# Kernel tuning notes

Hardware: AMD Instinct MI355X
Metric: run time of the kernel (lower is better)

Reference implementation:

```python
import jax, jax.numpy as jnp
import numpy as np

B, N, D = 16, 4096, 768   # bags, instances per bag, feature dim
H, L, K = 12, 2, 16       # heads, MHA layers, topk
DH = D // H               # head dim (also gate hidden dim)


def _ln(x, g, b, eps=1e-5):
    m = x.mean(-1, keepdims=True)
    v = x.var(-1, keepdims=True)
    return (x - m) / jnp.sqrt(v + eps) * g + b


def setup_inputs() -> dict:
    key = jax.random.key(0)
    ks = jax.random.split(key, 8)
    s = 0.02
    return {
        "x": jax.random.normal(ks[0], (B, N, D), jnp.float32),
        "cls_token": jax.random.normal(ks[1], (1, 1, D), jnp.float32),
        "ln_g": jnp.ones((D,), jnp.float32),
        "ln_b": jnp.zeros((D,), jnp.float32),
        "gln_g": jnp.ones((D,), jnp.float32),
        "gln_b": jnp.zeros((D,), jnp.float32),
        "gW1": jax.random.normal(ks[2], (DH, D), jnp.float32) * s,
        "gb1": jnp.zeros((DH,), jnp.float32),
        "gW2": jax.random.normal(ks[3], (1, DH), jnp.float32) * s,
        "gb2": jnp.zeros((1,), jnp.float32),
        "Wqkv": jax.random.normal(ks[4], (L, 3 * D, D), jnp.float32) * s,
        "bqkv": jnp.zeros((L, 3 * D), jnp.float32),
        "Wo": jax.random.normal(ks[5], (L, D, D), jnp.float32) * s,
        "bo": jnp.zeros((L, D), jnp.float32),
    }


def reference(x, cls_token, ln_g, ln_b, gln_g, gln_b, gW1, gb1, gW2, gb2, Wqkv, bqkv, Wo, bo):
    # --- per-bag attention gate: LN -> Linear(D,DH) -> GELU -> Linear(DH,1) -> sigmoid ---
    z = _ln(x, gln_g, gln_b)                                      # [B,N,D]
    h = jax.nn.gelu(jnp.einsum('bnd,ed->bne', z, gW1) + gb1, approximate=False)
    w = jax.nn.sigmoid((jnp.einsum('bne,oe->bno', h, gW2) + gb2)[..., 0])  # [B,N]
    # --- top-k selection (argsort descending, take first K) + gather + weight ---
    topv, topi = jax.lax.top_k(w, K)                              # [B,K]
    sel = jnp.take_along_axis(x, topi[..., None], axis=1) * topv[..., None]  # [B,K,D]
    # --- prepend cls token, shared LayerNorm ---
    cls = jnp.broadcast_to(cls_token, (B, 1, D))
    seq = jnp.concatenate([cls, sel], axis=1)                     # [B,K+1,D]
    z0 = _ln(seq, ln_g, ln_b)
    a = z0
    S = K + 1
    scale = 1.0 / jnp.sqrt(jnp.asarray(DH, jnp.float32))
    # --- stacked MHA; residual always from z0, shared ln (matches source) ---
    for l in range(L):
        qkv = jnp.einsum('bsd,ed->bse', a, Wqkv[l]) + bqkv[l]     # [B,S,3D]
        q, k, v = jnp.split(qkv, 3, axis=-1)
        q = q.reshape(B, S, H, DH)
        k = k.reshape(B, S, H, DH)
        v = v.reshape(B, S, H, DH)
        att = jax.nn.softmax(jnp.einsum('bqhd,bkhd->bhqk', q, k) * scale, axis=-1)
        o = jnp.einsum('bhqk,bkhd->bqhd', att, v).reshape(B, S, D)
        o = jnp.einsum('bsd,ed->bse', o, Wo[l]) + bo[l]
        a = _ln(z0 + o, ln_g, ln_b)
    # dropout is identity in eval mode
    return a[:, 0, :]                                             # [B,D]
```

## Files before the change

### kernel.cpp

```cpp
#include <hip/hip_runtime.h>
#include <hip/hip_bf16.h>
#include <math.h>

#define B_   16
#define N_   4096
#define D_   768
#define H_   12
#define L_   2
#define K_   16
#define S_   17
#define M_   272
#define BN_  65536

typedef __bf16 bf16x8 __attribute__((ext_vector_type(8)));
typedef float  f32x4  __attribute__((ext_vector_type(4)));

static __device__ __forceinline__ unsigned short f2bf(float f) {
    __bf16 h = (__bf16)f;
    return __builtin_bit_cast(unsigned short, h);
}
static __device__ __forceinline__ float bf2f(unsigned short u) {
    __bf16 h = __builtin_bit_cast(__bf16, u);
    return (float)h;
}
static __device__ __forceinline__ unsigned long long umax64(unsigned long long a, unsigned long long b) {
    return a > b ? a : b;
}
static __device__ __forceinline__ void split4(const float4& v, ushort4& hh, ushort4& ll) {
    hh.x = f2bf(v.x); ll.x = f2bf(v.x - bf2f(hh.x));
    hh.y = f2bf(v.y); ll.y = f2bf(v.y - bf2f(hh.y));
    hh.z = f2bf(v.z); ll.z = f2bf(v.z - bf2f(hh.z));
    hh.w = f2bf(v.w); ll.w = f2bf(v.w - bf2f(hh.w));
}

__global__ __launch_bounds__(256)
void gate_kernel(const float* __restrict__ x, const float* __restrict__ gln_g,
                 const float* __restrict__ gln_b, const float* __restrict__ gW1,
                 const float* __restrict__ gb1, const float* __restrict__ gW2,
                 const float* __restrict__ gb2, float* __restrict__ wbuf)
{
    __shared__ __align__(16) char WS[16384];
    __shared__ float mS[128], rS[128], A1s[64], A2s[64];
    __shared__ float rA1[256], rA2[256];
    char* WhB = WS;
    char* WlB = WS + 8192;

    const int t   = threadIdx.x;
    const int bn0 = blockIdx.x * 128;
    const int wv  = t >> 6, la = t & 63, fr = la & 15, fq = la >> 4;

    const int te = t >> 2;
    const int tq = (t & 3) * 16;
    const float* wrow = gW1 + (size_t)te * D_ + tq;

    const float* arow0 = x + (size_t)(bn0 + wv * 32 + fr) * D_;
    const float* arow1 = arow0 + (size_t)16 * D_;

    f32x4 acc[2][4];
    #pragma unroll
    for (int mi = 0; mi < 2; ++mi)
        #pragma unroll
        for (int ni = 0; ni < 4; ++ni) {
            f32x4 z = {0.f, 0.f, 0.f, 0.f};
            acc[mi][ni] = z;
        }

    float sx0 = 0.f, sxx0 = 0.f, sx1 = 0.f, sxx1 = 0.f;
    float a1p = 0.f, a2p = 0.f;

    float4 pa[2][2][2];
    #pragma unroll
    for (int mi = 0; mi < 2; ++mi) {
        const float* ar = mi ? arow1 : arow0;
        #pragma unroll
        for (int ks = 0; ks < 2; ++ks) {
            pa[mi][ks][0] = *(const float4*)(ar + ks * 32 + fq * 8);
            pa[mi][ks][1] = *(const float4*)(ar + ks * 32 + fq * 8 + 4);
        }
    }

    for (int kt = 0; kt < 12; ++kt) {
        __syncthreads();
        {
            const float* wsrc = wrow + kt * 64;
            const float* gsrc = gln_g + kt * 64 + tq;
            const float* bsrc = gln_b + kt * 64 + tq;
            #pragma unroll
            for (int j = 0; j < 4; ++j) {
                float4 w4 = *(const float4*)(wsrc + j * 4);
                float4 g4 = *(const float4*)(gsrc + j * 4);
                float4 b4 = *(const float4*)(bsrc + j * 4);
                float4 wt;
                wt.x = w4.x * g4.x; wt.y = w4.y * g4.y;
                wt.z = w4.z * g4.z; wt.w = w4.w * g4.w;
                a1p += wt.x + wt.y + wt.z + wt.w;
                a2p += b4.x * w4.x + b4.y * w4.y + b4.z * w4.z + b4.w * w4.w;
                ushort4 hh, ll;
                split4(wt, hh, ll);
                int byte = (te * 128 + (tq + j * 4) * 2) ^ ((te & 7) << 4);
                *(ushort4*)(WhB + byte) = hh;
                *(ushort4*)(WlB + byte) = ll;
            }
        }
        __syncthreads();

        float4 na[2][2][2];
        if (kt < 11) {
            #pragma unroll
            for (int mi = 0; mi < 2; ++mi) {
                const float* ar = (mi ? arow1 : arow0) + (kt + 1) * 64;
                #pragma unroll
                for (int ks = 0; ks < 2; ++ks) {
                    na[mi][ks][0] = *(const float4*)(ar + ks * 32 + fq * 8);
                    na[mi][ks][1] = *(const float4*)(ar + ks * 32 + fq * 8 + 4);
                }
            }
        }

        #pragma unroll
        for (int ks = 0; ks < 2; ++ks) {
            bf16x8 ah[2], al[2];
            #pragma unroll
            for (int mi = 0; mi < 2; ++mi) {
                float v[8];
                v[0] = pa[mi][ks][0].x; v[1] = pa[mi][ks][0].y;
                v[2] = pa[mi][ks][0].z; v[3] = pa[mi][ks][0].w;
                v[4] = pa[mi][ks][1].x; v[5] = pa[mi][ks][1].y;
                v[6] = pa[mi][ks][1].z; v[7] = pa[mi][ks][1].w;
                #pragma unroll
                for (int i = 0; i < 8; ++i) {
                    if (mi == 0) { sx0 += v[i]; sxx0 += v[i] * v[i]; }
                    else         { sx1 += v[i]; sxx1 += v[i] * v[i]; }
                    __bf16 h = (__bf16)v[i];
                    ah[mi][i] = h;
                    al[mi][i] = (__bf16)(v[i] - (float)h);
                }
            }
            bf16x8 bh[4], bl[4];
            const int kb = ks * 64 + fq * 16;
            #pragma unroll
            for (int ni = 0; ni < 4; ++ni) {
                int e    = ni * 16 + fr;
                int byte = (e * 128 + kb) ^ ((e & 7) << 4);
                bh[ni] = *(const bf16x8*)(WhB + byte);
                bl[ni] = *(const bf16x8*)(WlB + byte);
            }
            #pragma unroll
            for (int mi = 0; mi < 2; ++mi)
                #pragma unroll
                for (int ni = 0; ni < 4; ++ni) {
                    acc[mi][ni] = __builtin_amdgcn_mfma_f32_16x16x32_bf16(ah[mi], bh[ni], acc[mi][ni], 0, 0, 0);
                    acc[mi][ni] = __builtin_amdgcn_mfma_f32_16x16x32_bf16(ah[mi], bl[ni], acc[mi][ni], 0, 0, 0);
                    acc[mi][ni] = __builtin_amdgcn_mfma_f32_16x16x32_bf16(al[mi], bh[ni], acc[mi][ni], 0, 0, 0);
                }
        }
        if (kt < 11) {
            #pragma unroll
            for (int mi = 0; mi < 2; ++mi)
                #pragma unroll
                for (int ks = 0; ks < 2; ++ks) {
                    pa[mi][ks][0] = na[mi][ks][0];
                    pa[mi][ks][1] = na[mi][ks][1];
                }
        }
    }

    __syncthreads();
    {
        float s0 = sx0, q0 = sxx0, s1 = sx1, q1 = sxx1;
        s0 += __shfl_xor(s0, 16); s0 += __shfl_xor(s0, 32);
        q0 += __shfl_xor(q0, 16); q0 += __shfl_xor(q0, 32);
        s1 += __shfl_xor(s1, 16); s1 += __shfl_xor(s1, 32);
        q1 += __shfl_xor(q1, 16); q1 += __shfl_xor(q1, 32);
        if (fq == 0) {
            int r0 = wv * 32 + fr;
            float m0 = s0 * (1.0f / D_);
            mS[r0] = m0;
            rS[r0] = rsqrtf(q0 * (1.0f / D_) - m0 * m0 + 1e-5f);
            float m1 = s1 * (1.0f / D_);
            mS[r0 + 16] = m1;
            rS[r0 + 16] = rsqrtf(q1 * (1.0f / D_) - m1 * m1 + 1e-5f);
        }
    }
    rA1[te * 4 + (t & 3)] = a1p;
    rA2[te * 4 + (t & 3)] = a2p;
    __syncthreads();
    if (t < 64) {
        A1s[t] = rA1[t * 4] + rA1[t * 4 + 1] + rA1[t * 4 + 2] + rA1[t * 4 + 3];
        A2s[t] = rA2[t * 4] + rA2[t * 4 + 1] + rA2[t * 4 + 2] + rA2[t * 4 + 3];
    }
    __syncthreads();

    float w2v[4], a1v[4], a2b[4];
    #pragma unroll
    for (int ni = 0; ni < 4; ++ni) {
        int e = ni * 16 + fr;
        w2v[ni] = gW2[e];
        a1v[ni] = A1s[e];
        a2b[ni] = A2s[e] + gb1[e];
    }
    float gb2v = gb2[0];

    #pragma unroll
    for (int mi = 0; mi < 2; ++mi) {
        #pragma unroll
        for (int j = 0; j < 4; ++j) {
            int inst = wv * 32 + mi * 16 + fq * 4 + j;
            float m = mS[inst], rs = rS[inst];
            float tp = 0.f;
            #pragma unroll
            for (int ni = 0; ni < 4; ++ni) {
                float h  = rs * (acc[mi][ni][j] - m * a1v[ni]) + a2b[ni];
                float hg = 0.5f * h * (1.0f + erff(h * 0.70710678118654752f));
                tp = fmaf(hg, w2v[ni], tp);
            }
            tp += __shfl_xor(tp, 1);
            tp += __shfl_xor(tp, 2);
            tp += __shfl_xor(tp, 4);
            tp += __shfl_xor(tp, 8);
            if (fr == 0) wbuf[bn0 + inst] = 1.0f / (1.0f + expf(-(tp + gb2v)));
        }
    }
}

__global__ __launch_bounds__(256)
void topkbuild_kernel(const float* __restrict__ x, const float* __restrict__ cls,
                      const float* __restrict__ ln_g, const float* __restrict__ ln_b,
                      const float* __restrict__ wbuf, float* __restrict__ z0)
{
    __shared__ unsigned long long SB[40];
    __shared__ float sm[8];
    const int b = blockIdx.x, t = threadIdx.x;
    const int la = t & 63, wid = t >> 6;

    unsigned long long key[16];
    #pragma unroll
    for (int j = 0; j < 16; ++j) {
        int i = t + 256 * j;
        float v = wbuf[(size_t)b * N_ + i];
        key[j] = ((unsigned long long)__float_as_uint(v) << 12) | (unsigned long long)(4095 - i);
    }
    for (int k = 0; k < K_; ++k) {
        unsigned long long kk = key[0];
        #pragma unroll
        for (int j = 1; j < 16; ++j) kk = umax64(kk, key[j]);
        #pragma unroll
        for (int o = 1; o < 64; o <<= 1) kk = umax64(kk, (unsigned long long)__shfl_xor(kk, o));
        if (la == 0) SB[wid] = kk;
        __syncthreads();
        if (t == 0) {
            unsigned long long m = umax64(umax64(SB[0], SB[1]), umax64(SB[2], SB[3]));
            SB[8] = m;
            SB[16 + k] = m;
        }
        __syncthreads();
        unsigned long long m = SB[8];
        int wi = 4095 - (int)(m & 0xfffULL);
        #pragma unroll
        for (int j = 0; j < 16; ++j)
            if (wi == t + 256 * j) key[j] = 0ULL;
        __syncthreads();
    }

    for (int s = 0; s < S_; ++s) {
        float v[3];
        if (s == 0) {
            #pragma unroll
            for (int p = 0; p < 3; ++p) v[p] = cls[t + 256 * p];
        } else {
            unsigned long long m = SB[16 + s - 1];
            int   idx = 4095 - (int)(m & 0xfffULL);
            float tv  = __uint_as_float((unsigned int)(m >> 12));
            const float* row = &x[((size_t)b * N_ + idx) * D_];
            #pragma unroll
            for (int p = 0; p < 3; ++p) v[p] = row[t + 256 * p] * tv;
        }
        float sum = 0.f, ss = 0.f;
        #pragma unroll
        for (int p = 0; p < 3; ++p) { sum += v[p]; ss += v[p] * v[p]; }
        #pragma unroll
        for (int o = 32; o; o >>= 1) { sum += __shfl_down(sum, o); ss += __shfl_down(ss, o); }
        if (la == 0) { sm[wid * 2] = sum; sm[wid * 2 + 1] = ss; }
        __syncthreads();
        sum = sm[0] + sm[2] + sm[4] + sm[6];
        ss  = sm[1] + sm[3] + sm[5] + sm[7];
        __syncthreads();
        float m = sum * (1.0f / D_), rstd = rsqrtf(ss * (1.0f / D_) - m * m + 1e-5f);
        #pragma unroll
        for (int p = 0; p < 3; ++p) {
            int d = t + 256 * p;
            z0[((size_t)(b * S_ + s)) * D_ + d] = (v[p] - m) * rstd * ln_g[d] + ln_b[d];
        }
    }
}

__global__ __launch_bounds__(256)
void gemm_mfma(const float* __restrict__ A, const float* __restrict__ W,
               const float* __restrict__ bias, float* __restrict__ C, int N)
{
    __shared__ __align__(16) char SB[32768];
    char* AhB = SB;
    char* AlB = SB + 8192;
    char* WhB = SB + 16384;
    char* WlB = SB + 24576;

    const int t  = threadIdx.x;
    const int m0 = blockIdx.x * 64, n0 = blockIdx.y * 64;

    const int sr = t >> 2;
    const int sc = (t & 3) * 16;
    const int gm = m0 + sr;
    const bool aok = (gm < M_);
    const float* asrc = A + (size_t)gm * D_ + sc;
    const float* wsrc = W + (size_t)(n0 + sr) * D_ + sc;

    const int wv = t >> 6, la = t & 63;
    const int fr = la & 15, fq = la >> 4;
    const int wm = (wv & 1) * 32, wn = (wv >> 1) * 32;

    f32x4 acc[2][2];
    #pragma unroll
    for (int mi = 0; mi < 2; ++mi)
        #pragma unroll
        for (int ni = 0; ni < 2; ++ni) {
            f32x4 z = {0.f, 0.f, 0.f, 0.f};
            acc[mi][ni] = z;
        }

    float4 pa[4], pw[4];
    #pragma unroll
    for (int q = 0; q < 4; ++q) {
        pa[q] = aok ? *(const float4*)(asrc + q * 4) : make_float4(0.f, 0.f, 0.f, 0.f);
        pw[q] = *(const float4*)(wsrc + q * 4);
    }

    const int abyte0 = sr * 128 + sc * 2;
    const int asw0   = (abyte0)      ^ ((sr & 7) << 4);
    const int asw1   = (abyte0 + 16) ^ ((sr & 7) << 4);

    for (int kt = 0; kt < 12; ++kt) {
        __syncthreads();
        {
            ushort4 hh[4], ll[4];
            #pragma unroll
            for (int q = 0; q < 4; ++q) split4(pa[q], hh[q], ll[q]);
            *(ushort4*)(AhB + asw0)     = hh[0];
            *(ushort4*)(AhB + asw0 + 8) = hh[1];
            *(ushort4*)(AhB + asw1)     = hh[2];
            *(ushort4*)(AhB + asw1 + 8) = hh[3];
            *(ushort4*)(AlB + asw0)     = ll[0];
            *(ushort4*)(AlB + asw0 + 8) = ll[1];
            *(ushort4*)(AlB + asw1)     = ll[2];
            *(ushort4*)(AlB + asw1 + 8) = ll[3];
            #pragma unroll
            for (int q = 0; q < 4; ++q) split4(pw[q], hh[q], ll[q]);
            *(ushort4*)(WhB + asw0)     = hh[0];
            *(ushort4*)(WhB + asw0 + 8) = hh[1];
            *(ushort4*)(WhB + asw1)     = hh[2];
            *(ushort4*)(WhB + asw1 + 8) = hh[3];
            *(ushort4*)(WlB + asw0)     = ll[0];
            *(ushort4*)(WlB + asw0 + 8) = ll[1];
            *(ushort4*)(WlB + asw1)     = ll[2];
            *(ushort4*)(WlB + asw1 + 8) = ll[3];
        }
        __syncthreads();
        if (kt < 11) {
            const float* an  = asrc + (kt + 1) * 64;
            const float* wn2 = wsrc + (kt + 1) * 64;
            #pragma unroll
            for (int q = 0; q < 4; ++q) {
                pa[q] = aok ? *(const float4*)(an + q * 4) : make_float4(0.f, 0.f, 0.f, 0.f);
                pw[q] = *(const float4*)(wn2 + q * 4);
            }
        }
        #pragma unroll
        for (int ks = 0; ks < 2; ++ks) {
            int kb = ks * 64 + fq * 16;
            bf16x8 ah[2], al[2], bh[2], bl[2];
            #pragma unroll
            for (int mi = 0; mi < 2; ++mi) {
                int r    = wm + mi * 16 + fr;
                int byte = (r * 128 + kb) ^ ((r & 7) << 4);
                ah[mi] = *(const bf16x8*)(AhB + byte);
                al[mi] = *(const bf16x8*)(AlB + byte);
            }
            #pragma unroll
            for (int ni = 0; ni < 2; ++ni) {
                int r    = wn + ni * 16 + fr;
                int byte = (r * 128 + kb) ^ ((r & 7) << 4);
                bh[ni] = *(const bf16x8*)(WhB + byte);
                bl[ni] = *(const bf16x8*)(WlB + byte);
            }
            #pragma unroll
            for (int mi = 0; mi < 2; ++mi)
                #pragma unroll
                for (int ni = 0; ni < 2; ++ni) {
                    acc[mi][ni] = __builtin_amdgcn_mfma_f32_16x16x32_bf16(ah[mi], bh[ni], acc[mi][ni], 0, 0, 0);
                    acc[mi][ni] = __builtin_amdgcn_mfma_f32_16x16x32_bf16(ah[mi], bl[ni], acc[mi][ni], 0, 0, 0);
                    acc[mi][ni] = __builtin_amdgcn_mfma_f32_16x16x32_bf16(al[mi], bh[ni], acc[mi][ni], 0, 0, 0);
                }
        }
    }

    #pragma unroll
    for (int mi = 0; mi < 2; ++mi) {
        #pragma unroll
        for (int j = 0; j < 4; ++j) {
            int m = m0 + wm + mi * 16 + fq * 4 + j;
            if (m < M_) {
                #pragma unroll
                for (int ni = 0; ni < 2; ++ni) {
                    int n = n0 + wn + ni * 16 + fr;
                    C[(size_t)m * N + n] = acc[mi][ni][j] + bias[n];
                }
            }
        }
    }
}

__global__ __launch_bounds__(256)
void attn_kernel(const float* __restrict__ qkvb, float* __restrict__ obuf)
{
    __shared__ __align__(16) float F[3 * S_ * 65 + S_ * 18];
    float* qs  = F;
    float* ks  = F + S_ * 65;
    float* vs  = F + 2 * S_ * 65;
    float* att = F + 3 * S_ * 65;
    const int bh = blockIdx.x, b = bh / H_, h = bh % H_;
    const int bq = b * S_;
    const int t = threadIdx.x;

    for (int idx = t; idx < S_ * 64; idx += 256) {
        int s = idx >> 6, d = idx & 63;
        size_t off = (size_t)(bq + s) * (3 * D_) + h * 64 + d;
        qs[s * 65 + d] = qkvb[off];
        ks[s * 65 + d] = qkvb[off + D_];
        vs[s * 65 + d] = qkvb[off + 2 * D_];
    }
    __syncthreads();
    for (int idx = t; idx < S_ * S_; idx += 256) {
        int i = idx / S_, j = idx % S_;
        float sdot = 0.f;
        #pragma unroll
        for (int d = 0; d < 64; ++d) sdot = fmaf(qs[i * 65 + d], ks[j * 65 + d], sdot);
        att[i * 18 + j] = sdot * 0.125f;
    }
    __syncthreads();
    if (t < S_) {
        float mx = -1e30f;
        for (int j = 0; j < S_; ++j) mx = fmaxf(mx, att[t * 18 + j]);
        float ssum = 0.f;
        for (int j = 0; j < S_; ++j) { float e = expf(att[t * 18 + j] - mx); att[t * 18 + j] = e; ssum += e; }
        float inv = 1.0f / ssum;
        for (int j = 0; j < S_; ++j) att[t * 18 + j] *= inv;
    }
    __syncthreads();
    for (int idx = t; idx < S_ * 64; idx += 256) {
        int i = idx >> 6, d = idx & 63;
        float s = 0.f;
        #pragma unroll
        for (int j = 0; j < S_; ++j) s = fmaf(att[i * 18 + j], vs[j * 65 + d], s);
        obuf[(size_t)(bq + i) * D_ + h * 64 + d] = s;
    }
}

__global__ __launch_bounds__(256)
void resln_kernel(const float* __restrict__ z0, const float* __restrict__ projb,
                  const float* __restrict__ ln_g, const float* __restrict__ ln_b,
                  float* __restrict__ abuf)
{
    __shared__ float sm[8];
    const int r = blockIdx.x, t = threadIdx.x;
    float v[3];
    #pragma unroll
    for (int p = 0; p < 3; ++p) {
        int d = t + 256 * p;
        v[p] = z0[(size_t)r * D_ + d] + projb[(size_t)r * D_ + d];
    }
    float sum = 0.f, ss = 0.f;
    #pragma unroll
    for (int p = 0; p < 3; ++p) { sum += v[p]; ss += v[p] * v[p]; }
    #pragma unroll
    for (int o = 32; o; o >>= 1) { sum += __shfl_down(sum, o); ss += __shfl_down(ss, o); }
    int wid = t >> 6, la = t & 63;
    if (la == 0) { sm[wid * 2] = sum; sm[wid * 2 + 1] = ss; }
    __syncthreads();
    sum = sm[0] + sm[2] + sm[4] + sm[6];
    ss  = sm[1] + sm[3] + sm[5] + sm[7];
    float m = sum * (1.0f / D_), rstd = rsqrtf(ss * (1.0f / D_) - m * m + 1e-5f);
    #pragma unroll
    for (int p = 0; p < 3; ++p) {
        int d = t + 256 * p;
        abuf[(size_t)r * D_ + d] = (v[p] - m) * rstd * ln_g[d] + ln_b[d];
    }
}

__global__ __launch_bounds__(256)
void outln_kernel(const float* __restrict__ z0, const float* __restrict__ projb,
                  const float* __restrict__ ln_g, const float* __restrict__ ln_b,
                  float* __restrict__ out)
{
    __shared__ float sm[8];
    const int b = blockIdx.x, t = threadIdx.x;
    const size_t r = (size_t)b * S_;
    float v[3];
    #pragma unroll
    for (int p = 0; p < 3; ++p) {
        int d = t + 256 * p;
        v[p] = z0[r * D_ + d] + projb[r * D_ + d];
    }
    float sum = 0.f, ss = 0.f;
    #pragma unroll
    for (int p = 0; p < 3; ++p) { sum += v[p]; ss += v[p] * v[p]; }
    #pragma unroll
    for (int o = 32; o; o >>= 1) { sum += __shfl_down(sum, o); ss += __shfl_down(ss, o); }
    int wid = t >> 6, la = t & 63;
    if (la == 0) { sm[wid * 2] = sum; sm[wid * 2 + 1] = ss; }
    __syncthreads();
    sum = sm[0] + sm[2] + sm[4] + sm[6];
    ss  = sm[1] + sm[3] + sm[5] + sm[7];
    float m = sum * (1.0f / D_), rstd = rsqrtf(ss * (1.0f / D_) - m * m + 1e-5f);
    #pragma unroll
    for (int p = 0; p < 3; ++p) {
        int d = t + 256 * p;
        out[(size_t)b * D_ + d] = (v[p] - m) * rstd * ln_g[d] + ln_b[d];
    }
}

extern "C" void kernel_launch(void* const* d_in, const int* in_sizes, int n_in,
                              void* d_out, int out_size, void* d_ws, size_t ws_size,
                              hipStream_t stream)
{
    const float* x     = (const float*)d_in[0];
    const float* cls   = (const float*)d_in[1];
    const float* ln_g  = (const float*)d_in[2];
    const float* ln_b  = (const float*)d_in[3];
    const float* gln_g = (const float*)d_in[4];
    const float* gln_b = (const float*)d_in[5];
    const float* gW1   = (const float*)d_in[6];
    const float* gb1   = (const float*)d_in[7];
    const float* gW2   = (const float*)d_in[8];
    const float* gb2   = (const float*)d_in[9];
    const float* Wqkv  = (const float*)d_in[10];
    const float* bqkv  = (const float*)d_in[11];
    const float* Wo    = (const float*)d_in[12];
    const float* bo    = (const float*)d_in[13];
    float* out = (float*)d_out;

    float* ws    = (float*)d_ws;
    float* wbuf  = ws;
    float* z0    = ws + BN_;
    float* abuf  = z0 + (size_t)M_ * D_;
    float* qkvb  = abuf + (size_t)M_ * D_;
    float* obuf  = qkvb + (size_t)M_ * 3 * D_;
    float* projb = obuf + (size_t)M_ * D_;

    gate_kernel<<<BN_ / 128, 256, 0, stream>>>(x, gln_g, gln_b, gW1, gb1, gW2, gb2, wbuf);
    topkbuild_kernel<<<B_, 256, 0, stream>>>(x, cls, ln_g, ln_b, wbuf, z0);

    gemm_mfma<<<dim3(5, 36), 256, 0, stream>>>(z0, Wqkv, bqkv, qkvb, 3 * D_);
    attn_kernel<<<B_ * H_, 256, 0, stream>>>(qkvb, obuf);
    gemm_mfma<<<dim3(5, 12), 256, 0, stream>>>(obuf, Wo, bo, projb, D_);
    resln_kernel<<<M_, 256, 0, stream>>>(z0, projb, ln_g, ln_b, abuf);

    gemm_mfma<<<dim3(5, 36), 256, 0, stream>>>(abuf, Wqkv + (size_t)3 * D_ * D_,
                                               bqkv + 3 * D_, qkvb, 3 * D_);
    attn_kernel<<<B_ * H_, 256, 0, stream>>>(qkvb, obuf);
    gemm_mfma<<<dim3(5, 12), 256, 0, stream>>>(obuf, Wo + (size_t)D_ * D_, bo + D_, projb, D_);
    outln_kernel<<<B_, 256, 0, stream>>>(z0, projb, ln_g, ln_b, out);
}
```

Baseline: 171.4 us.

## Precompute gate weight split once and compute only CLS row in final layer

A new single-block prep kernel folds the gate LayerNorm gamma into gW1, splits the result into bf16 hi/lo pairs in a global swizzled layout, and reduces the A1/A2 bias terms once. Before, each of 512 gate blocks redid this conversion for every k-tile, and the gate kernel now just copies the prepared tiles into LDS. In the last layer only the CLS query row goes through attention, and a small 16-row projection kernel replaces the full Wo GEMM, since only a[:,0,:] is returned. The cost is an extra tiny kernel launch, plus the second-layer QKV GEMM still computing all rows.

```diff
diff --git a/kernel.cpp b/kernel.cpp
--- a/kernel.cpp
+++ b/kernel.cpp
@@ -34,25 +34,50 @@
 }
 
 __global__ __launch_bounds__(256)
-void gate_kernel(const float* __restrict__ x, const float* __restrict__ gln_g,
-                 const float* __restrict__ gln_b, const float* __restrict__ gW1,
+void prep_kernel(const float* __restrict__ gln_g, const float* __restrict__ gln_b,
+                 const float* __restrict__ gW1,
+                 char* __restrict__ wsh, char* __restrict__ wsl,
+                 float* __restrict__ A1g, float* __restrict__ A2g)
+{
+    const int t = threadIdx.x;
+    const int e = t >> 2;
+    const int c0 = (t & 3) * 192;
+    float a1 = 0.f, a2 = 0.f;
+    for (int c = c0; c < c0 + 192; c += 4) {
+        float4 w = *(const float4*)&gW1[(size_t)e * D_ + c];
+        float4 g = *(const float4*)&gln_g[c];
+        float4 bb = *(const float4*)&gln_b[c];
+        float4 wt;
+        wt.x = w.x * g.x; wt.y = w.y * g.y; wt.z = w.z * g.z; wt.w = w.w * g.w;
+        a1 += wt.x + wt.y + wt.z + wt.w;
+        a2 += bb.x * w.x + bb.y * w.y + bb.z * w.z + bb.w * w.w;
+        ushort4 hh, ll;
+        split4(wt, hh, ll);
+        int kt = c >> 6, cc = c & 63;
+        int byte = (e * 128 + cc * 2) ^ ((e & 7) << 4);
+        *(ushort4*)(wsh + kt * 8192 + byte) = hh;
+        *(ushort4*)(wsl + kt * 8192 + byte) = ll;
+    }
+    a1 += __shfl_xor(a1, 1); a1 += __shfl_xor(a1, 2);
+    a2 += __shfl_xor(a2, 1); a2 += __shfl_xor(a2, 2);
+    if ((t & 3) == 0) { A1g[e] = a1; A2g[e] = a2; }
+}
+
+__global__ __launch_bounds__(256)
+void gate_kernel(const float* __restrict__ x,
+                 const char* __restrict__ wsh, const char* __restrict__ wsl,
+                 const float* __restrict__ A1g, const float* __restrict__ A2g,
                  const float* __restrict__ gb1, const float* __restrict__ gW2,
                  const float* __restrict__ gb2, float* __restrict__ wbuf)
 {
-    __shared__ __align__(16) char WS[16384];
-    __shared__ float mS[128], rS[128], A1s[64], A2s[64];
-    __shared__ float rA1[256], rA2[256];
-    char* WhB = WS;
-    char* WlB = WS + 8192;
+    __shared__ __align__(16) char WhS[8192];
+    __shared__ __align__(16) char WlS[8192];
+    __shared__ float mS[128], rS[128];
 
     const int t   = threadIdx.x;
     const int bn0 = blockIdx.x * 128;
     const int wv  = t >> 6, la = t & 63, fr = la & 15, fq = la >> 4;
 
-    const int te = t >> 2;
-    const int tq = (t & 3) * 16;
-    const float* wrow = gW1 + (size_t)te * D_ + tq;
-
     const float* arow0 = x + (size_t)(bn0 + wv * 32 + fr) * D_;
     const float* arow1 = arow0 + (size_t)16 * D_;
 
@@ -66,7 +91,6 @@
         }
 
     float sx0 = 0.f, sxx0 = 0.f, sx1 = 0.f, sxx1 = 0.f;
-    float a1p = 0.f, a2p = 0.f;
 
     float4 pa[2][2][2];
     #pragma unroll
@@ -78,30 +102,17 @@
             pa[mi][ks][1] = *(const float4*)(ar + ks * 32 + fq * 8 + 4);
         }
     }
+    uint4 pwh0 = *(const uint4*)(wsh + t * 16);
+    uint4 pwh1 = *(const uint4*)(wsh + t * 16 + 4096);
+    uint4 pwl0 = *(const uint4*)(wsl + t * 16);
+    uint4 pwl1 = *(const uint4*)(wsl + t * 16 + 4096);
 
     for (int kt = 0; kt < 12; ++kt) {
         __syncthreads();
-        {
-            const float* wsrc = wrow + kt * 64;
-            const float* gsrc = gln_g + kt * 64 + tq;
-            const float* bsrc = gln_b + kt * 64 + tq;
-            #pragma unroll
-            for (int j = 0; j < 4; ++j) {
-                float4 w4 = *(const float4*)(wsrc + j * 4);
-                float4 g4 = *(const float4*)(gsrc + j * 4);
-                float4 b4 = *(const float4*)(bsrc + j * 4);
-                float4 wt;
-                wt.x = w4.x * g4.x; wt.y = w4.y * g4.y;
-                wt.z = w4.z * g4.z; wt.w = w4.w * g4.w;
-                a1p += wt.x + wt.y + wt.z + wt.w;
-                a2p += b4.x * w4.x + b4.y * w4.y + b4.z * w4.z + b4.w * w4.w;
-                ushort4 hh, ll;
-                split4(wt, hh, ll);
-                int byte = (te * 128 + (tq + j * 4) * 2) ^ ((te & 7) << 4);
-                *(ushort4*)(WhB + byte) = hh;
-                *(ushort4*)(WlB + byte) = ll;
-            }
-        }
+        *(uint4*)(WhS + t * 16)        = pwh0;
+        *(uint4*)(WhS + t * 16 + 4096) = pwh1;
+        *(uint4*)(WlS + t * 16)        = pwl0;
+        *(uint4*)(WlS + t * 16 + 4096) = pwl1;
         __syncthreads();
 
         float4 na[2][2][2];
@@ -115,6 +126,12 @@
                     na[mi][ks][1] = *(const float4*)(ar + ks * 32 + fq * 8 + 4);
                 }
             }
+            const char* wb = wsh + (kt + 1) * 8192 + t * 16;
+            const char* lb = wsl + (kt + 1) * 8192 + t * 16;
+            pwh0 = *(const uint4*)(wb);
+            pwh1 = *(const uint4*)(wb + 4096);
+            pwl0 = *(const uint4*)(lb);
+            pwl1 = *(const uint4*)(lb + 4096);
         }
 
         #pragma unroll
@@ -142,8 +159,8 @@
             for (int ni = 0; ni < 4; ++ni) {
                 int e    = ni * 16 + fr;
                 int byte = (e * 128 + kb) ^ ((e & 7) << 4);
-                bh[ni] = *(const bf16x8*)(WhB + byte);
-                bl[ni] = *(const bf16x8*)(WlB + byte);
+                bh[ni] = *(const bf16x8*)(WhS + byte);
+                bl[ni] = *(const bf16x8*)(WlS + byte);
             }
             #pragma unroll
             for (int mi = 0; mi < 2; ++mi)
@@ -182,13 +199,6 @@
             rS[r0 + 16] = rsqrtf(q1 * (1.0f / D_) - m1 * m1 + 1e-5f);
         }
     }
-    rA1[te * 4 + (t & 3)] = a1p;
-    rA2[te * 4 + (t & 3)] = a2p;
-    __syncthreads();
-    if (t < 64) {
-        A1s[t] = rA1[t * 4] + rA1[t * 4 + 1] + rA1[t * 4 + 2] + rA1[t * 4 + 3];
-        A2s[t] = rA2[t * 4] + rA2[t * 4 + 1] + rA2[t * 4 + 2] + rA2[t * 4 + 3];
-    }
     __syncthreads();
 
     float w2v[4], a1v[4], a2b[4];
@@ -196,8 +206,8 @@
     for (int ni = 0; ni < 4; ++ni) {
         int e = ni * 16 + fr;
         w2v[ni] = gW2[e];
-        a1v[ni] = A1s[e];
-        a2b[ni] = A2s[e] + gb1[e];
+        a1v[ni] = A1g[e];
+        a2b[ni] = A2g[e] + gb1[e];
     }
     float gb2v = gb2[0];
 
@@ -495,19 +505,146 @@
     }
 }
 
+__global__ __launch_bounds__(128)
+void attn1r0_kernel(const float* __restrict__ qkvb, float* __restrict__ o1c)
+{
+    __shared__ float q0[64], kv[S_][65], vv[S_][64], p[S_], red[2];
+    const int bh = blockIdx.x, b = bh / H_, h = bh % H_;
+    const int t = threadIdx.x;
+    const size_t rowbase = (size_t)(b * S_) * (3 * D_) + h * 64;
+
+    for (int idx = t; idx < S_ * 64; idx += 128) {
+        int s = idx >> 6, d = idx & 63;
+        kv[s][d] = qkvb[rowbase + (size_t)s * (3 * D_) + D_ + d];
+        vv[s][d] = qkvb[rowbase + (size_t)s * (3 * D_) + 2 * D_ + d];
+    }
+    if (t < 64) q0[t] = qkvb[rowbase + t];
+    __syncthreads();
+    if (t < S_) {
+        float sdot = 0.f;
+        #pragma unroll
+        for (int d = 0; d < 64; ++d) sdot = fmaf(q0[d], kv[t][d], sdot);
+        p[t] = sdot * 0.125f;
+    }
+    __syncthreads();
+    if (t == 0) {
+        float mx = -1e30f;
+        for (int j = 0; j < S_; ++j) mx = fmaxf(mx, p[j]);
+        red[0] = mx;
+    }
+    __syncthreads();
+    if (t < S_) p[t] = expf(p[t] - red[0]);
+    __syncthreads();
+    if (t == 0) {
+        float s = 0.f;
+        for (int j = 0; j < S_; ++j) s += p[j];
+        red[1] = 1.0f / s;
+    }
+    __syncthreads();
+    if (t < 64) {
+        float s = 0.f;
+        #pragma unroll
+        for (int j = 0; j < S_; ++j) s = fmaf(p[j], vv[j][t], s);
+        o1c[(size_t)b * D_ + h * 64 + t] = s * red[1];
+    }
+}
+
 __global__ __launch_bounds__(256)
-void outln_kernel(const float* __restrict__ z0, const float* __restrict__ projb,
+void proj1c_kernel(const float* __restrict__ A,
+                   const float* __restrict__ W,
+                   const float* __restrict__ bias,
+                   float* __restrict__ C)
+{
+    __shared__ __align__(16) char SB[20480];
+    char* AhB = SB;
+    char* AlB = SB + 2048;
+    char* WhB = SB + 4096;
+    char* WlB = SB + 12288;
+
+    const int t  = threadIdx.x;
+    const int n0 = blockIdx.x * 64;
+
+    const int ar = t >> 4;
+    const int ac = (t & 15) * 4;
+    const int sr = t >> 2;
+    const int sc = (t & 3) * 16;
+
+    const int wv = t >> 6, la = t & 63;
+    const int fr = la & 15, fq = la >> 4;
+
+    f32x4 acc = {0.f, 0.f, 0.f, 0.f};
+
+    float4 pa = *(const float4*)(A + (size_t)ar * D_ + ac);
+    float4 pw[4];
+    #pragma unroll
+    for (int q = 0; q < 4; ++q)
+        pw[q] = *(const float4*)(W + (size_t)(n0 + sr) * D_ + sc + q * 4);
+
+    for (int kt = 0; kt < 12; ++kt) {
+        __syncthreads();
+        {
+            ushort4 hh, ll;
+            split4(pa, hh, ll);
+            int byte = (ar * 128 + ac * 2) ^ ((ar & 7) << 4);
+            *(ushort4*)(AhB + byte) = hh;
+            *(ushort4*)(AlB + byte) = ll;
+            ushort4 whh[4], wll[4];
+            #pragma unroll
+            for (int q = 0; q < 4; ++q) split4(pw[q], whh[q], wll[q]);
+            int wb0 = (sr * 128 + sc * 2) ^ ((sr & 7) << 4);
+            int wb1 = (sr * 128 + sc * 2 + 16) ^ ((sr & 7) << 4);
+            *(ushort4*)(WhB + wb0)     = whh[0];
+            *(ushort4*)(WhB + wb0 + 8) = whh[1];
+            *(ushort4*)(WhB + wb1)     = whh[2];
+            *(ushort4*)(WhB + wb1 + 8) = whh[3];
+            *(ushort4*)(WlB + wb0)     = wll[0];
+            *(ushort4*)(WlB + wb0 + 8) = wll[1];
+            *(ushort4*)(WlB + wb1)     = wll[2];
+            *(ushort4*)(WlB + wb1 + 8) = wll[3];
+        }
+        __syncthreads();
+        if (kt < 11) {
+            pa = *(const float4*)(A + (size_t)ar * D_ + (kt + 1) * 64 + ac);
+            #pragma unroll
+            for (int q = 0; q < 4; ++q)
+                pw[q] = *(const float4*)(W + (size_t)(n0 + sr) * D_ + (kt + 1) * 64 + sc + q * 4);
+        }
+        #pragma unroll
+        for (int ks = 0; ks < 2; ++ks) {
+            int kb = ks * 64 + fq * 16;
+            int abyte = (fr * 128 + kb) ^ ((fr & 7) << 4);
+            bf16x8 ah = *(const bf16x8*)(AhB + abyte);
+            bf16x8 al = *(const bf16x8*)(AlB + abyte);
+            int r = wv * 16 + fr;
+            int wbyte = (r * 128 + kb) ^ ((r & 7) << 4);
+            bf16x8 bh = *(const bf16x8*)(WhB + wbyte);
+            bf16x8 bl = *(const bf16x8*)(WlB + wbyte);
+            acc = __builtin_amdgcn_mfma_f32_16x16x32_bf16(ah, bh, acc, 0, 0, 0);
+            acc = __builtin_amdgcn_mfma_f32_16x16x32_bf16(ah, bl, acc, 0, 0, 0);
+            acc = __builtin_amdgcn_mfma_f32_16x16x32_bf16(al, bh, acc, 0, 0, 0);
+        }
+    }
+
+    #pragma unroll
+    for (int j = 0; j < 4; ++j) {
+        int m = fq * 4 + j;
+        int n = n0 + wv * 16 + fr;
+        C[(size_t)m * D_ + n] = acc[j] + bias[n];
+    }
+}
+
+__global__ __launch_bounds__(256)
+void outln_kernel(const float* __restrict__ z0, const float* __restrict__ projc,
                   const float* __restrict__ ln_g, const float* __restrict__ ln_b,
                   float* __restrict__ out)
 {
     __shared__ float sm[8];
     const int b = blockIdx.x, t = threadIdx.x;
-    const size_t r = (size_t)b * S_;
     float v[3];
     #pragma unroll
     for (int p = 0; p < 3; ++p) {
         int d = t + 256 * p;
-        v[p] = z0[r * D_ + d] + projb[r * D_ + d];
+        v[p] = z0[((size_t)b * S_) * D_ + d] + projc[(size_t)b * D_ + d];
     }
     float sum = 0.f, ss = 0.f;
     #pragma unroll
@@ -554,8 +691,14 @@
     float* qkvb  = abuf + (size_t)M_ * D_;
     float* obuf  = qkvb + (size_t)M_ * 3 * D_;
     float* projb = obuf + (size_t)M_ * D_;
-
-    gate_kernel<<<BN_ / 128, 256, 0, stream>>>(x, gln_g, gln_b, gW1, gb1, gW2, gb2, wbuf);
+    float* A1g   = projb + (size_t)M_ * D_;
+    float* A2g   = A1g + 64;
+    char*  wsh   = (char*)(A2g + 64);
+    wsh = (char*)(((uintptr_t)wsh + 15) & ~(uintptr_t)15);
+    char*  wsl   = wsh + 12 * 8192;
+
+    prep_kernel<<<1, 256, 0, stream>>>(gln_g, gln_b, gW1, wsh, wsl, A1g, A2g);
+    gate_kernel<<<BN_ / 128, 256, 0, stream>>>(x, wsh, wsl, A1g, A2g, gb1, gW2, gb2, wbuf);
     topkbuild_kernel<<<B_, 256, 0, stream>>>(x, cls, ln_g, ln_b, wbuf, z0);
 
     gemm_mfma<<<dim3(5, 36), 256, 0, stream>>>(z0, Wqkv, bqkv, qkvb, 3 * D_);
@@ -565,7 +708,7 @@
 
     gemm_mfma<<<dim3(5, 36), 256, 0, stream>>>(abuf, Wqkv + (size_t)3 * D_ * D_,
                                                bqkv + 3 * D_, qkvb, 3 * D_);
-    attn_kernel<<<B_ * H_, 256, 0, stream>>>(qkvb, obuf);
-    gemm_mfma<<<dim3(5, 12), 256, 0, stream>>>(obuf, Wo + (size_t)D_ * D_, bo + D_, projb, D_);
+    attn1r0_kernel<<<B_ * H_, 128, 0, stream>>>(qkvb, obuf);
+    proj1c_kernel<<<12, 256, 0, stream>>>(obuf, Wo + (size_t)D_ * D_, bo + D_, projb);
     outln_kernel<<<B_, 256, 0, stream>>>(z0, projb, ln_g, ln_b, out);
 }
```

Measured after the change: 191.7 us. +11.8%, slower.
